# Kernel tuning notes

Measured on AMD Instinct MI355X. Metric: run time of the kernel, lower is better.

Reference implementation:

```python
import jax, jax.numpy as jnp
import numpy as np

S, B, D, H = 2048, 2, 1024, 16
DH = D // H
WINDOW = 256
DILATION = 1


def setup_inputs() -> dict:
    key = jax.random.key(0)
    ks = jax.random.split(key, 10)
    scale = 1.0 / np.sqrt(D)
    x = jax.random.normal(ks[0], (S, B, D), dtype=jnp.float32)
    Wq = jax.random.normal(ks[1], (D, D), dtype=jnp.float32) * scale
    Wk = jax.random.normal(ks[2], (D, D), dtype=jnp.float32) * scale
    Wv = jax.random.normal(ks[3], (D, D), dtype=jnp.float32) * scale
    Wo = jax.random.normal(ks[4], (D, D), dtype=jnp.float32) * scale
    bq = jax.random.normal(ks[5], (D,), dtype=jnp.float32) * 0.01
    bk = jax.random.normal(ks[6], (D,), dtype=jnp.float32) * 0.01
    bv = jax.random.normal(ks[7], (D,), dtype=jnp.float32) * 0.01
    bo = jax.random.normal(ks[8], (D,), dtype=jnp.float32) * 0.01
    beta = jax.random.normal(ks[9], (H,), dtype=jnp.float32) * 0.1
    return {"x": x, "Wq": Wq, "bq": bq, "Wk": Wk, "bk": bk,
            "Wv": Wv, "bv": bv, "Wo": Wo, "bo": bo, "beta": beta}


def _causal_window_bias(seq_len, window_len, dilation):
    # allowed iff 0 <= i-j <= dilation*(window_len-1) and (i-j) % dilation == 0
    idx = jnp.arange(seq_len)
    diff = idx[:, None] - idx[None, :]
    allowed = (diff >= 0) & (diff <= dilation * (window_len - 1)) & (diff % dilation == 0)
    return jnp.where(allowed, 0.0, -jnp.inf).astype(jnp.float32)  # [S, S]


def reference(x, Wq, bq, Wk, bk, Wv, bv, Wo, bo, beta):
    s, b, d = x.shape
    # projections (torch Linear: x @ W.T + b)
    q = x @ Wq.T + bq
    k = x @ Wk.T + bk
    v = x @ Wv.T + bv
    # 's b (h d) -> b h s d'
    q = q.reshape(s, b, H, DH).transpose(1, 2, 0, 3)
    k = k.reshape(s, b, H, DH).transpose(1, 2, 0, 3)
    v = v.reshape(s, b, H, DH).transpose(1, 2, 0, 3)
    # per-head beta scaling: q / (sqrt(d_head) * exp(beta))
    q = q / (np.sqrt(DH) * jnp.exp(beta)[None, :, None, None])
    bias = _causal_window_bias(s, WINDOW, DILATION)  # [S, S]
    scores = jnp.einsum('bhqd,bhkd->bhqk', q, k) + bias[None, None]
    p = jax.nn.softmax(scores, axis=-1)
    out = jnp.einsum('bhqk,bhkd->bhqd', p, v)
    # 'b h s d -> s b (h d)'
    out = out.transpose(2, 0, 1, 3).reshape(s, b, d)
    return out @ Wo.T + bo
```

## Files before the change

kernel.cpp:

```cpp
#include <hip/hip_runtime.h>
#include <hip/hip_bf16.h>

#define S_LEN 2048
#define BATCH 2
#define DMODEL 1024
#define NHEAD 16
#define DHEAD 64
#define WINDOW 256
#define MROWS (S_LEN * BATCH)

typedef unsigned short u16;
typedef unsigned int u32;
typedef __attribute__((ext_vector_type(8))) short bf16x8;
typedef __attribute__((ext_vector_type(4))) float f32x4;
typedef __attribute__((ext_vector_type(2))) unsigned int u32x2;

typedef const __attribute__((address_space(1))) void gvoid;
typedef __attribute__((address_space(3))) void lvoid;

__device__ __forceinline__ float b2f(u16 u) {
    union { unsigned int i; float f; } x; x.i = ((unsigned int)u) << 16; return x.f;
}
__device__ __forceinline__ u16 f2b(float f) {
    union { float f; unsigned int i; } x; x.f = f;
    unsigned int r = x.i + 0x7fffu + ((x.i >> 16) & 1u);
    return (u16)(r >> 16);
}
__device__ __forceinline__ u32 cvtpk(float a, float b) {
    u32 r; asm("v_cvt_pk_bf16_f32 %0, %1, %2" : "=v"(r) : "v"(a), "v"(b)); return r;
}
__device__ __forceinline__ bf16x8 ld8f(const float* __restrict__ p) {
    bf16x8 r;
    #pragma unroll
    for (int i = 0; i < 8; i++) r[i] = (short)f2b(p[i]);
    return r;
}
template<bool BF>
__device__ __forceinline__ bf16x8 ldrow(const void* __restrict__ base, size_t elemOff) {
    if constexpr (BF) return *reinterpret_cast<const bf16x8*>((const u16*)base + elemOff);
    else              return ld8f((const float*)base + elemOff);
}

__global__ __launch_bounds__(256) void cast_all(
    const float* __restrict__ x,  const float* __restrict__ Wq,
    const float* __restrict__ Wk, const float* __restrict__ Wv,
    const float* __restrict__ Wo,
    u16* __restrict__ xb, u16* __restrict__ wb, u16* __restrict__ wob)
{
    const size_t idx = ((size_t)blockIdx.x * 256 + threadIdx.x) * 8;
    const size_t M1 = 1048576;
    const float* src; u16* dst;
    if (idx < 4 * M1)      { src = x  + idx;            dst = xb  + idx; }
    else if (idx < 5 * M1) { src = Wq + (idx - 4 * M1); dst = wb  + (idx - 4 * M1); }
    else if (idx < 6 * M1) { src = Wk + (idx - 5 * M1); dst = wb  + (idx - 4 * M1); }
    else if (idx < 7 * M1) { src = Wv + (idx - 6 * M1); dst = wb  + (idx - 4 * M1); }
    else                   { src = Wo + (idx - 7 * M1); dst = wob + (idx - 7 * M1); }
    *reinterpret_cast<bf16x8*>(dst) = ld8f(src);
}

__global__ __launch_bounds__(256) void gemm_qkv_s(
    const u16* __restrict__ A, const u16* __restrict__ Wall,
    const float* __restrict__ bq, const float* __restrict__ bk, const float* __restrict__ bv,
    const float* __restrict__ beta,
    u16* __restrict__ qbuf, u16* __restrict__ kbuf, u16* __restrict__ vt)
{
    __shared__ u16 lA[128 * 32];
    __shared__ u16 lB[128 * 32];
    const int tid = threadIdx.x;
    const int lane = tid & 63, wave = tid >> 6;
    const int r15 = lane & 15, g = lane >> 4;
    const int m0 = blockIdx.x * 128;
    const int range = blockIdx.y >> 3;
    const int n0 = (blockIdx.y & 7) * 128;
    const u16* W = Wall + (size_t)range * DMODEL * DMODEL;
    const float* bias = (range == 0) ? bq : (range == 1) ? bk : bv;

    const int srow = tid >> 2;
    const int sslot = (tid & 3) ^ ((tid >> 3) & 3);
    const u16* aSrc = A + (size_t)(m0 + srow) * DMODEL + sslot * 8;
    const u16* wSrc = W + (size_t)(n0 + srow) * DMODEL + sslot * 8;
    const int ldsW = wave * 1024;
    const int mrow = (wave >> 1) * 64, nrow = (wave & 1) * 64;
    const int swz = (g ^ ((r15 >> 1) & 3)) << 4;
    const char* lAr = (const char*)lA + swz;
    const char* lBr = (const char*)lB + swz;

    f32x4 acc[4][4] = {};
    for (int kk = 0; kk < DMODEL; kk += 32) {
        __syncthreads();
        #pragma unroll
        for (int ro = 0; ro < 2; ro++) {
            __builtin_amdgcn_global_load_lds(
                (gvoid*)(aSrc + (size_t)ro * 64 * DMODEL + kk),
                (lvoid*)((char*)lA + ro * 4096 + ldsW), 16, 0, 0);
            __builtin_amdgcn_global_load_lds(
                (gvoid*)(wSrc + (size_t)ro * 64 * DMODEL + kk),
                (lvoid*)((char*)lB + ro * 4096 + ldsW), 16, 0, 0);
        }
        __syncthreads();
        bf16x8 af[4], bf[4];
        #pragma unroll
        for (int mi = 0; mi < 4; mi++)
            af[mi] = *reinterpret_cast<const bf16x8*>(lAr + ((mrow + mi * 16 + r15) << 6));
        #pragma unroll
        for (int ni = 0; ni < 4; ni++)
            bf[ni] = *reinterpret_cast<const bf16x8*>(lBr + ((nrow + ni * 16 + r15) << 6));
        #pragma unroll
        for (int mi = 0; mi < 4; mi++)
            #pragma unroll
            for (int ni = 0; ni < 4; ni++)
                acc[mi][ni] = __builtin_amdgcn_mfma_f32_16x16x32_bf16(
                    af[mi], bf[ni], acc[mi][ni], 0, 0, 0);
    }
    #pragma unroll
    for (int ni = 0; ni < 4; ni++) {
        const int col = n0 + nrow + ni * 16 + r15;
        const float bv_ = bias[col];
        float scale = 1.0f;
        if (range == 0) scale = 1.0f / (8.0f * __expf(beta[col >> 6]));
        #pragma unroll
        for (int mi = 0; mi < 4; mi++)
            #pragma unroll
            for (int r = 0; r < 4; r++) {
                const int row = m0 + mrow + mi * 16 + g * 4 + r;
                const float val = acc[mi][ni][r] + bv_;
                if (range == 0) {
                    qbuf[(size_t)row * DMODEL + col] = f2b(val * scale);
                } else if (range == 1) {
                    kbuf[(size_t)row * DMODEL + col] = f2b(val);
                } else {
                    const int b = row & 1, s = row >> 1;
                    vt[((size_t)(b * NHEAD + (col >> 6)) * DHEAD + (col & 63)) * S_LEN + s]
                        = f2b(val);
                }
            }
    }
}

__global__ __launch_bounds__(256) void gemm_out_s(
    const u16* __restrict__ A, const u16* __restrict__ W,
    const float* __restrict__ bias, float* __restrict__ C)
{
    __shared__ u16 lA[128 * 32];
    __shared__ u16 lB[128 * 32];
    const int tid = threadIdx.x;
    const int lane = tid & 63, wave = tid >> 6;
    const int r15 = lane & 15, g = lane >> 4;
    const int m0 = blockIdx.x * 128;
    const int n0 = blockIdx.y * 128;

    const int srow = tid >> 2;
    const int sslot = (tid & 3) ^ ((tid >> 3) & 3);
    const u16* aSrc = A + (size_t)(m0 + srow) * DMODEL + sslot * 8;
    const u16* wSrc = W + (size_t)(n0 + srow) * DMODEL + sslot * 8;
    const int ldsW = wave * 1024;
    const int mrow = (wave >> 1) * 64, nrow = (wave & 1) * 64;
    const int swz = (g ^ ((r15 >> 1) & 3)) << 4;
    const char* lAr = (const char*)lA + swz;
    const char* lBr = (const char*)lB + swz;

    f32x4 acc[4][4] = {};
    for (int kk = 0; kk < DMODEL; kk += 32) {
        __syncthreads();
        #pragma unroll
        for (int ro = 0; ro < 2; ro++) {
            __builtin_amdgcn_global_load_lds(
                (gvoid*)(aSrc + (size_t)ro * 64 * DMODEL + kk),
                (lvoid*)((char*)lA + ro * 4096 + ldsW), 16, 0, 0);
            __builtin_amdgcn_global_load_lds(
                (gvoid*)(wSrc + (size_t)ro * 64 * DMODEL + kk),
                (lvoid*)((char*)lB + ro * 4096 + ldsW), 16, 0, 0);
        }
        __syncthreads();
        bf16x8 af[4], bf[4];
        #pragma unroll
        for (int mi = 0; mi < 4; mi++)
            af[mi] = *reinterpret_cast<const bf16x8*>(lAr + ((mrow + mi * 16 + r15) << 6));
        #pragma unroll
        for (int ni = 0; ni < 4; ni++)
            bf[ni] = *reinterpret_cast<const bf16x8*>(lBr + ((nrow + ni * 16 + r15) << 6));
        #pragma unroll
        for (int mi = 0; mi < 4; mi++)
            #pragma unroll
            for (int ni = 0; ni < 4; ni++)
                acc[mi][ni] = __builtin_amdgcn_mfma_f32_16x16x32_bf16(
                    af[mi], bf[ni], acc[mi][ni], 0, 0, 0);
    }
    #pragma unroll
    for (int ni = 0; ni < 4; ni++) {
        const int col = n0 + nrow + ni * 16 + r15;
        const float bv_ = bias[col];
        #pragma unroll
        for (int mi = 0; mi < 4; mi++)
            #pragma unroll
            for (int r = 0; r < 4; r++) {
                const int row = m0 + mrow + mi * 16 + g * 4 + r;
                C[(size_t)row * DMODEL + col] = acc[mi][ni][r] + bv_;
            }
    }
}

template<bool ABF, bool WBF>
__global__ __launch_bounds__(256) void gemm_qkv_t(
    const void* __restrict__ A_,
    const void* __restrict__ Wq_, const void* __restrict__ Wk_, const void* __restrict__ Wv_,
    const float* __restrict__ bq, const float* __restrict__ bk, const float* __restrict__ bv,
    const float* __restrict__ beta,
    u16* __restrict__ qbuf, u16* __restrict__ kbuf, u16* __restrict__ vt)
{
    const int lane = threadIdx.x & 63;
    const int wave = threadIdx.x >> 6;
    const int r15 = lane & 15, g = lane >> 4;
    const int m0 = blockIdx.x * 128 + (wave >> 1) * 64;
    const int range = blockIdx.y >> 3;
    const int n0 = (blockIdx.y & 7) * 128 + (wave & 1) * 64;
    const void* W_ = (range == 0) ? Wq_ : (range == 1) ? Wk_ : Wv_;
    const float* bias = (range == 0) ? bq : (range == 1) ? bk : bv;
    const size_t aBase = (size_t)(m0 + r15) * DMODEL + g * 8;
    const size_t wBase = (size_t)(n0 + r15) * DMODEL + g * 8;
    f32x4 acc[4][4] = {};
    for (int k = 0; k < DMODEL; k += 32) {
        bf16x8 af[4], bf[4];
        #pragma unroll
        for (int mi = 0; mi < 4; mi++) af[mi] = ldrow<ABF>(A_, aBase + (size_t)mi * 16 * DMODEL + k);
        #pragma unroll
        for (int ni = 0; ni < 4; ni++) bf[ni] = ldrow<WBF>(W_, wBase + (size_t)ni * 16 * DMODEL + k);
        #pragma unroll
        for (int mi = 0; mi < 4; mi++)
            #pragma unroll
            for (int ni = 0; ni < 4; ni++)
                acc[mi][ni] = __builtin_amdgcn_mfma_f32_16x16x32_bf16(
                    af[mi], bf[ni], acc[mi][ni], 0, 0, 0);
    }
    #pragma unroll
    for (int ni = 0; ni < 4; ni++) {
        const int col = n0 + ni * 16 + r15;
        const float bv_ = bias[col];
        float scale = 1.0f;
        if (range == 0) scale = 1.0f / (8.0f * __expf(beta[col >> 6]));
        #pragma unroll
        for (int mi = 0; mi < 4; mi++)
            #pragma unroll
            for (int r = 0; r < 4; r++) {
                const int row = m0 + mi * 16 + g * 4 + r;
                const float val = acc[mi][ni][r] + bv_;
                if (range == 0) {
                    qbuf[(size_t)row * DMODEL + col] = f2b(val * scale);
                } else if (range == 1) {
                    kbuf[(size_t)row * DMODEL + col] = f2b(val);
                } else {
                    const int b = row & 1, s = row >> 1;
                    vt[((size_t)(b * NHEAD + (col >> 6)) * DHEAD + (col & 63)) * S_LEN + s]
                        = f2b(val);
                }
            }
    }
}

template<bool WBF>
__global__ __launch_bounds__(256) void gemm_out_t(
    const u16* __restrict__ A, const void* __restrict__ W_,
    const float* __restrict__ bias, float* __restrict__ C)
{
    const int lane = threadIdx.x & 63;
    const int wave = threadIdx.x >> 6;
    const int r15 = lane & 15, g = lane >> 4;
    const int m0 = blockIdx.x * 64 + (wave >> 1) * 32;
    const int n0 = blockIdx.y * 128 + (wave & 1) * 64;
    const u16* a0 = A + (size_t)(m0 + r15) * DMODEL + g * 8;
    const size_t wBase = (size_t)(n0 + r15) * DMODEL + g * 8;
    f32x4 acc[2][4] = {};
    for (int k = 0; k < DMODEL; k += 32) {
        bf16x8 af[2], bf[4];
        #pragma unroll
        for (int mi = 0; mi < 2; mi++)
            af[mi] = *reinterpret_cast<const bf16x8*>(a0 + (size_t)mi * 16 * DMODEL + k);
        #pragma unroll
        for (int ni = 0; ni < 4; ni++) bf[ni] = ldrow<WBF>(W_, wBase + (size_t)ni * 16 * DMODEL + k);
        #pragma unroll
        for (int mi = 0; mi < 2; mi++)
            #pragma unroll
            for (int ni = 0; ni < 4; ni++)
                acc[mi][ni] = __builtin_amdgcn_mfma_f32_16x16x32_bf16(
                    af[mi], bf[ni], acc[mi][ni], 0, 0, 0);
    }
    #pragma unroll
    for (int ni = 0; ni < 4; ni++) {
        const int col = n0 + ni * 16 + r15;
        const float bv_ = bias[col];
        #pragma unroll
        for (int mi = 0; mi < 2; mi++)
            #pragma unroll
            for (int r = 0; r < 4; r++) {
                const int row = m0 + mi * 16 + g * 4 + r;
                C[(size_t)row * DMODEL + col] = acc[mi][ni][r] + bv_;
            }
    }
}

__global__ __launch_bounds__(256) void attn3(
    const u16* __restrict__ qb, const u16* __restrict__ kb_,
    const u16* __restrict__ vt, u16* __restrict__ O)
{
    __shared__ u16 plds[4][16][64];
    const int lane = threadIdx.x & 63;
    const int wave = threadIdx.x >> 6;
    const int bid  = blockIdx.x;
    const int sbid = (bid & 7) * 128 + (bid >> 3);
    const int wid = sbid * 4 + wave;
    const int qt = wid & (S_LEN / 16 - 1);
    const int h  = (wid >> 7) & (NHEAD - 1);
    const int b  = wid >> 11;
    const int qstart = qt * 16;
    const int r15 = lane & 15, g = lane >> 4;
    const int i_glob = qstart + r15;

    const u16* qrow = qb + ((size_t)i_glob * BATCH + b) * DMODEL + h * DHEAD;
    const bf16x8 qf0 = *reinterpret_cast<const bf16x8*>(qrow + g * 8);
    const bf16x8 qf1 = *reinterpret_cast<const bf16x8*>(qrow + 32 + g * 8);
    const u16* vbase = vt + (size_t)(b * NHEAD + h) * DHEAD * S_LEN;

    char* prow = (char*)plds + wave * 2048 + r15 * 128;
    const int q7 = r15 & 7;

    float psum = 0.0f;
    f32x4 o[4] = {};
    const int kt0 = (qstart >= WINDOW) ? (qstart - WINDOW) : 0;

    for (int kt = kt0; kt <= qstart; kt += 64) {
        bf16x8 ka[4], kc[4];
        #pragma unroll
        for (int t = 0; t < 4; t++) {
            const int kr = min(kt + t * 16 + r15, S_LEN - 1);
            const u16* kp = kb_ + ((size_t)kr * BATCH + b) * DMODEL + h * DHEAD;
            ka[t] = *reinterpret_cast<const bf16x8*>(kp + g * 8);
            kc[t] = *reinterpret_cast<const bf16x8*>(kp + 32 + g * 8);
        }
        f32x4 st[4] = {};
        #pragma unroll
        for (int t = 0; t < 4; t++) {
            st[t] = __builtin_amdgcn_mfma_f32_16x16x32_bf16(ka[t], qf0, st[t], 0, 0, 0);
            st[t] = __builtin_amdgcn_mfma_f32_16x16x32_bf16(kc[t], qf1, st[t], 0, 0, 0);
        }

        #pragma unroll
        for (int t = 0; t < 4; t++) {
            float p[4];
            #pragma unroll
            for (int r = 0; r < 4; r++) {
                const int j = kt + t * 16 + g * 4 + r;
                const int d = i_glob - j;
                p[r] = (d < 0 || d >= WINDOW) ? 0.0f : __expf(st[t][r]);
                psum += p[r];
            }
            u32x2 w;
            w.x = cvtpk(p[0], p[1]);
            w.y = cvtpk(p[2], p[3]);
            *reinterpret_cast<u32x2*>(
                prow + ((((t << 1) + (g >> 1)) ^ q7) << 4) + ((g & 1) << 3)) = w;
        }

        const bf16x8 pf0 = *reinterpret_cast<const bf16x8*>(prow + ((g ^ q7) << 4));
        const bf16x8 pf1 = *reinterpret_cast<const bf16x8*>(prow + (((4 + g) ^ q7) << 4));

        int s0 = kt + g * 8;       if (s0 >= S_LEN) s0 = 0;
        int s1 = kt + 32 + g * 8;  if (s1 >= S_LEN) s1 = 0;
        #pragma unroll
        for (int c = 0; c < 4; c++) {
            const u16* vr = vbase + (size_t)(c * 16 + r15) * S_LEN;
            const bf16x8 vf0 = *reinterpret_cast<const bf16x8*>(vr + s0);
            const bf16x8 vf1 = *reinterpret_cast<const bf16x8*>(vr + s1);
            o[c] = __builtin_amdgcn_mfma_f32_16x16x32_bf16(vf0, pf0, o[c], 0, 0, 0);
            o[c] = __builtin_amdgcn_mfma_f32_16x16x32_bf16(vf1, pf1, o[c], 0, 0, 0);
        }
    }

    psum += __shfl_xor(psum, 16);
    psum += __shfl_xor(psum, 32);
    const float inv = 1.0f / psum;
    #pragma unroll
    for (int c = 0; c < 4; c++)
        #pragma unroll
        for (int r = 0; r < 4; r++) {
            const int dh = c * 16 + g * 4 + r;
            O[((size_t)i_glob * BATCH + b) * DMODEL + h * DHEAD + dh] = f2b(o[c][r] * inv);
        }
}

extern "C" void kernel_launch(void* const* d_in, const int* in_sizes, int n_in,
                              void* d_out, int out_size, void* d_ws, size_t ws_size,
                              hipStream_t stream) {
    const float* x    = (const float*)d_in[0];
    const float* Wq   = (const float*)d_in[1];
    const float* bq   = (const float*)d_in[2];
    const float* Wk   = (const float*)d_in[3];
    const float* bk   = (const float*)d_in[4];
    const float* Wv   = (const float*)d_in[5];
    const float* bv   = (const float*)d_in[6];
    const float* Wo   = (const float*)d_in[7];
    const float* bo   = (const float*)d_in[8];
    const float* beta = (const float*)d_in[9];
    float* out = (float*)d_out;
    u16* ws = (u16*)d_ws;

    const size_t M4 = (size_t)MROWS * DMODEL;
    u16* qbuf = (u16*)d_out;
    u16* kbuf = (u16*)d_out + M4;
    u16* vtb  = ws;
    u16* abuf = ws + M4;

    const int nattn = BATCH * NHEAD * (S_LEN / 16) / 4;
    dim3 gqkv(MROWS / 128, 24);
    dim3 gout(MROWS / 128, 8);

    if (ws_size >= (size_t)32 * 1024 * 1024) {
        u16* xb  = ws + 2 * M4;
        u16* wb  = ws + 3 * M4;
        u16* wob = ws + 3 * M4 + 3145728;
        cast_all<<<4096, 256, 0, stream>>>(x, Wq, Wk, Wv, Wo, xb, wb, wob);
        gemm_qkv_s<<<gqkv, 256, 0, stream>>>(xb, wb, bq, bk, bv, beta, qbuf, kbuf, vtb);
        attn3<<<nattn, 256, 0, stream>>>(qbuf, kbuf, vtb, abuf);
        gemm_out_s<<<gout, 256, 0, stream>>>(abuf, wob, bo, out);
    } else {
        dim3 gout2(MROWS / 64, 8);
        gemm_qkv_t<false, false><<<gqkv, 256, 0, stream>>>(
            x, Wq, Wk, Wv, bq, bk, bv, beta, qbuf, kbuf, vtb);
        attn3<<<nattn, 256, 0, stream>>>(qbuf, kbuf, vtb, abuf);
        gemm_out_t<false><<<gout2, 256, 0, stream>>>(abuf, Wo, bo, out);
    }
}
```

Before: 111.4 us.

## Split each attention query tile's key window across two waves and reduce via LDS

The attention kernel now assigns two waves to each 16-row query tile. Each wave processes up to three 64-key chunks of the 256-key window, and the partial outputs and softmax sums are combined through shared memory. This doubles the number of waves and shortens the serial per-wave loop to raise parallelism and latency hiding. In exchange it adds a block-wide barrier, an LDS reduction and extra clamped loads. An occupancy hint is also added to launch bounds.

After: 122.5 us. 1.1x slower.

```diff
diff --git a/kernel.cpp b/kernel.cpp
--- a/kernel.cpp
+++ b/kernel.cpp
@@ -298,19 +298,22 @@
     }
 }
 
-__global__ __launch_bounds__(256) void attn3(
+__global__ __launch_bounds__(256, 6) void attn4(
     const u16* __restrict__ qb, const u16* __restrict__ kb_,
     const u16* __restrict__ vt, u16* __restrict__ O)
 {
     __shared__ u16 plds[4][16][64];
+    __shared__ float ored[2][64][17];
     const int lane = threadIdx.x & 63;
     const int wave = threadIdx.x >> 6;
     const int bid  = blockIdx.x;
-    const int sbid = (bid & 7) * 128 + (bid >> 3);
-    const int wid = sbid * 4 + wave;
-    const int qt = wid & (S_LEN / 16 - 1);
-    const int h  = (wid >> 7) & (NHEAD - 1);
-    const int b  = wid >> 11;
+    const int sbid = (bid & 7) * 256 + (bid >> 3);
+    const int wid2 = sbid * 4 + wave;
+    const int half = wid2 & 1;
+    const int pair = wid2 >> 1;
+    const int qt = pair & (S_LEN / 16 - 1);
+    const int h  = (pair >> 7) & (NHEAD - 1);
+    const int b  = pair >> 11;
     const int qstart = qt * 16;
     const int r15 = lane & 15, g = lane >> 4;
     const int i_glob = qstart + r15;
@@ -325,66 +328,81 @@
 
     float psum = 0.0f;
     f32x4 o[4] = {};
-    const int kt0 = (qstart >= WINDOW) ? (qstart - WINDOW) : 0;
-
-    for (int kt = kt0; kt <= qstart; kt += 64) {
-        bf16x8 ka[4], kc[4];
-        #pragma unroll
-        for (int t = 0; t < 4; t++) {
-            const int kr = min(kt + t * 16 + r15, S_LEN - 1);
-            const u16* kp = kb_ + ((size_t)kr * BATCH + b) * DMODEL + h * DHEAD;
-            ka[t] = *reinterpret_cast<const bf16x8*>(kp + g * 8);
-            kc[t] = *reinterpret_cast<const bf16x8*>(kp + 32 + g * 8);
+
+    #pragma unroll
+    for (int i = 0; i < 3; i++) {
+        const int cs = qstart - WINDOW + (half * 3 + i) * 64;
+        if (cs >= -63 && cs <= qstart) {
+            bf16x8 ka[4], kc[4];
+            #pragma unroll
+            for (int t = 0; t < 4; t++) {
+                const int kr = min(max(cs + t * 16 + r15, 0), S_LEN - 1);
+                const u16* kp = kb_ + ((size_t)kr * BATCH + b) * DMODEL + h * DHEAD;
+                ka[t] = *reinterpret_cast<const bf16x8*>(kp + g * 8);
+                kc[t] = *reinterpret_cast<const bf16x8*>(kp + 32 + g * 8);
+            }
+            f32x4 st[4] = {};
+            #pragma unroll
+            for (int t = 0; t < 4; t++) {
+                st[t] = __builtin_amdgcn_mfma_f32_16x16x32_bf16(ka[t], qf0, st[t], 0, 0, 0);
+                st[t] = __builtin_amdgcn_mfma_f32_16x16x32_bf16(kc[t], qf1, st[t], 0, 0, 0);
+            }
+            #pragma unroll
+            for (int t = 0; t < 4; t++) {
+                float p[4];
+                #pragma unroll
+                for (int r = 0; r < 4; r++) {
+                    const int j = cs + t * 16 + g * 4 + r;
+                    const int d = i_glob - j;
+                    p[r] = (j < 0 || d < 0 || d >= WINDOW) ? 0.0f : __expf(st[t][r]);
+                    psum += p[r];
+                }
+                u32x2 w;
+                w.x = cvtpk(p[0], p[1]);
+                w.y = cvtpk(p[2], p[3]);
+                *reinterpret_cast<u32x2*>(
+                    prow + ((((t << 1) + (g >> 1)) ^ q7) << 4) + ((g & 1) << 3)) = w;
+            }
+            const bf16x8 pf0 = *reinterpret_cast<const bf16x8*>(prow + ((g ^ q7) << 4));
+            const bf16x8 pf1 = *reinterpret_cast<const bf16x8*>(prow + (((4 + g) ^ q7) << 4));
+            const int s0 = min(max(cs + g * 8, 0), S_LEN - 8);
+            const int s1 = min(max(cs + 32 + g * 8, 0), S_LEN - 8);
+            #pragma unroll
+            for (int c = 0; c < 4; c++) {
+                const u16* vr = vbase + (size_t)(c * 16 + r15) * S_LEN;
+                const bf16x8 vf0 = *reinterpret_cast<const bf16x8*>(vr + s0);
+                const bf16x8 vf1 = *reinterpret_cast<const bf16x8*>(vr + s1);
+                o[c] = __builtin_amdgcn_mfma_f32_16x16x32_bf16(vf0, pf0, o[c], 0, 0, 0);
+                o[c] = __builtin_amdgcn_mfma_f32_16x16x32_bf16(vf1, pf1, o[c], 0, 0, 0);
+            }
         }
-        f32x4 st[4] = {};
-        #pragma unroll
-        for (int t = 0; t < 4; t++) {
-            st[t] = __builtin_amdgcn_mfma_f32_16x16x32_bf16(ka[t], qf0, st[t], 0, 0, 0);
-            st[t] = __builtin_amdgcn_mfma_f32_16x16x32_bf16(kc[t], qf1, st[t], 0, 0, 0);
-        }
-
-        #pragma unroll
-        for (int t = 0; t < 4; t++) {
-            float p[4];
+    }
+
+    if (half) {
+        #pragma unroll
+        for (int c = 0; c < 4; c++)
+            #pragma unroll
+            for (int r = 0; r < 4; r++) ored[wave >> 1][lane][c * 4 + r] = o[c][r];
+        ored[wave >> 1][lane][16] = psum;
+    }
+    __syncthreads();
+    if (!half) {
+        #pragma unroll
+        for (int c = 0; c < 4; c++)
+            #pragma unroll
+            for (int r = 0; r < 4; r++) o[c][r] += ored[wave >> 1][lane][c * 4 + r];
+        psum += ored[wave >> 1][lane][16];
+        psum += __shfl_xor(psum, 16);
+        psum += __shfl_xor(psum, 32);
+        const float inv = 1.0f / psum;
+        #pragma unroll
+        for (int c = 0; c < 4; c++)
             #pragma unroll
             for (int r = 0; r < 4; r++) {
-                const int j = kt + t * 16 + g * 4 + r;
-                const int d = i_glob - j;
-                p[r] = (d < 0 || d >= WINDOW) ? 0.0f : __expf(st[t][r]);
-                psum += p[r];
-            }
-            u32x2 w;
-            w.x = cvtpk(p[0], p[1]);
-            w.y = cvtpk(p[2], p[3]);
-            *reinterpret_cast<u32x2*>(
-                prow + ((((t << 1) + (g >> 1)) ^ q7) << 4) + ((g & 1) << 3)) = w;
-        }
-
-        const bf16x8 pf0 = *reinterpret_cast<const bf16x8*>(prow + ((g ^ q7) << 4));
-        const bf16x8 pf1 = *reinterpret_cast<const bf16x8*>(prow + (((4 + g) ^ q7) << 4));
-
-        int s0 = kt + g * 8;       if (s0 >= S_LEN) s0 = 0;
-        int s1 = kt + 32 + g * 8;  if (s1 >= S_LEN) s1 = 0;
-        #pragma unroll
-        for (int c = 0; c < 4; c++) {
-            const u16* vr = vbase + (size_t)(c * 16 + r15) * S_LEN;
-            const bf16x8 vf0 = *reinterpret_cast<const bf16x8*>(vr + s0);
-            const bf16x8 vf1 = *reinterpret_cast<const bf16x8*>(vr + s1);
-            o[c] = __builtin_amdgcn_mfma_f32_16x16x32_bf16(vf0, pf0, o[c], 0, 0, 0);
-            o[c] = __builtin_amdgcn_mfma_f32_16x16x32_bf16(vf1, pf1, o[c], 0, 0, 0);
-        }
-    }
-
-    psum += __shfl_xor(psum, 16);
-    psum += __shfl_xor(psum, 32);
-    const float inv = 1.0f / psum;
-    #pragma unroll
-    for (int c = 0; c < 4; c++)
-        #pragma unroll
-        for (int r = 0; r < 4; r++) {
-            const int dh = c * 16 + g * 4 + r;
-            O[((size_t)i_glob * BATCH + b) * DMODEL + h * DHEAD + dh] = f2b(o[c][r] * inv);
-        }
+                const int dh = c * 16 + g * 4 + r;
+                O[((size_t)i_glob * BATCH + b) * DMODEL + h * DHEAD + dh] = f2b(o[c][r] * inv);
+            }
+    }
 }
 
 extern "C" void kernel_launch(void* const* d_in, const int* in_sizes, int n_in,
@@ -409,7 +427,7 @@
     u16* vtb  = ws;
     u16* abuf = ws + M4;
 
-    const int nattn = BATCH * NHEAD * (S_LEN / 16) / 4;
+    const int nattn = BATCH * NHEAD * (S_LEN / 16) * 2 / 4;
     dim3 gqkv(MROWS / 128, 24);
     dim3 gout(MROWS / 128, 8);
 
@@ -419,13 +437,13 @@
         u16* wob = ws + 3 * M4 + 3145728;
         cast_all<<<4096, 256, 0, stream>>>(x, Wq, Wk, Wv, Wo, xb, wb, wob);
         gemm_qkv_s<<<gqkv, 256, 0, stream>>>(xb, wb, bq, bk, bv, beta, qbuf, kbuf, vtb);
-        attn3<<<nattn, 256, 0, stream>>>(qbuf, kbuf, vtb, abuf);
+        attn4<<<nattn, 256, 0, stream>>>(qbuf, kbuf, vtb, abuf);
         gemm_out_s<<<gout, 256, 0, stream>>>(abuf, wob, bo, out);
     } else {
         dim3 gout2(MROWS / 64, 8);
         gemm_qkv_t<false, false><<<gqkv, 256, 0, stream>>>(
             x, Wq, Wk, Wv, bq, bk, bv, beta, qbuf, kbuf, vtb);
-        attn3<<<nattn, 256, 0, stream>>>(qbuf, kbuf, vtb, abuf);
+        attn4<<<nattn, 256, 0, stream>>>(qbuf, kbuf, vtb, abuf);
         gemm_out_t<false><<<gout2, 256, 0, stream>>>(abuf, Wo, bo, out);
     }
 }
```

## Swizzle global bf16 layouts across all stages and double-buffer attention P tile

Applied to the files above, without the earlier changes.

Applies an XOR swizzle on 128-element chunks, keyed by row, to the global layouts of the bf16 x/weights, Q, K, V^T and the attention output. Every producer and consumer kernel is updated to match, so row-strided global accesses are spread across memory channels instead of colliding. The attention P scratch in LDS is also double-buffered by key-tile parity, which may relax the ordering between writing and reading P. The cost is extra index math and a layout coupling that every stage must keep consistent. The non-workspace fallback path keeps the unswizzled layout.

New measurement: 132.2 us. 18.7% more time.

```diff
diff --git a/kernel.cpp b/kernel.cpp
--- a/kernel.cpp
+++ b/kernel.cpp
@@ -49,14 +49,16 @@
 {
     const size_t idx = ((size_t)blockIdx.x * 256 + threadIdx.x) * 8;
     const size_t M1 = 1048576;
+    const size_t sw = ((idx >> 10) & 7) << 7;
     const float* src; u16* dst;
-    if (idx < 4 * M1)      { src = x  + idx;            dst = xb  + idx; }
-    else if (idx < 5 * M1) { src = Wq + (idx - 4 * M1); dst = wb  + (idx - 4 * M1); }
-    else if (idx < 6 * M1) { src = Wk + (idx - 5 * M1); dst = wb  + (idx - 4 * M1); }
-    else if (idx < 7 * M1) { src = Wv + (idx - 6 * M1); dst = wb  + (idx - 4 * M1); }
-    else                   { src = Wo + (idx - 7 * M1); dst = wob + (idx - 7 * M1); }
+    if (idx < 4 * M1)      { src = x  + idx;            dst = xb  + ((idx)          ^ sw); }
+    else if (idx < 5 * M1) { src = Wq + (idx - 4 * M1); dst = wb  + ((idx - 4 * M1) ^ sw); }
+    else if (idx < 6 * M1) { src = Wk + (idx - 5 * M1); dst = wb  + ((idx - 4 * M1) ^ sw); }
+    else if (idx < 7 * M1) { src = Wv + (idx - 6 * M1); dst = wb  + ((idx - 4 * M1) ^ sw); }
+    else                   { src = Wo + (idx - 7 * M1); dst = wob + ((idx - 7 * M1) ^ sw); }
     *reinterpret_cast<bf16x8*>(dst) = ld8f(src);
 }
+
 
 __global__ __launch_bounds__(256) void gemm_qkv_s(
     const u16* __restrict__ A, const u16* __restrict__ Wall,
@@ -77,6 +79,7 @@
 
     const int srow = tid >> 2;
     const int sslot = (tid & 3) ^ ((tid >> 3) & 3);
+    const int arswz = ((srow & 7) << 7);
     const u16* aSrc = A + (size_t)(m0 + srow) * DMODEL + sslot * 8;
     const u16* wSrc = W + (size_t)(n0 + srow) * DMODEL + sslot * 8;
     const int ldsW = wave * 1024;
@@ -87,14 +90,15 @@
 
     f32x4 acc[4][4] = {};
     for (int kk = 0; kk < DMODEL; kk += 32) {
+        const int kks = kk ^ arswz;
         __syncthreads();
         #pragma unroll
         for (int ro = 0; ro < 2; ro++) {
             __builtin_amdgcn_global_load_lds(
-                (gvoid*)(aSrc + (size_t)ro * 64 * DMODEL + kk),
+                (gvoid*)(aSrc + (size_t)ro * 64 * DMODEL + kks),
                 (lvoid*)((char*)lA + ro * 4096 + ldsW), 16, 0, 0);
             __builtin_amdgcn_global_load_lds(
-                (gvoid*)(wSrc + (size_t)ro * 64 * DMODEL + kk),
+                (gvoid*)(wSrc + (size_t)ro * 64 * DMODEL + kks),
                 (lvoid*)((char*)lB + ro * 4096 + ldsW), 16, 0, 0);
         }
         __syncthreads();
@@ -123,15 +127,16 @@
             #pragma unroll
             for (int r = 0; r < 4; r++) {
                 const int row = m0 + mrow + mi * 16 + g * 4 + r;
+                const int s = row >> 1;
                 const float val = acc[mi][ni][r] + bv_;
                 if (range == 0) {
-                    qbuf[(size_t)row * DMODEL + col] = f2b(val * scale);
+                    qbuf[(size_t)row * DMODEL + (col ^ ((s & 7) << 7))] = f2b(val * scale);
                 } else if (range == 1) {
-                    kbuf[(size_t)row * DMODEL + col] = f2b(val);
+                    kbuf[(size_t)row * DMODEL + (col ^ ((s & 7) << 7))] = f2b(val);
                 } else {
-                    const int b = row & 1, s = row >> 1;
-                    vt[((size_t)(b * NHEAD + (col >> 6)) * DHEAD + (col & 63)) * S_LEN + s]
-                        = f2b(val);
+                    const int b = row & 1;
+                    vt[((size_t)(b * NHEAD + (col >> 6)) * DHEAD + (col & 63)) * S_LEN
+                       + (s ^ ((col & 7) << 7))] = f2b(val);
                 }
             }
     }
@@ -151,6 +156,7 @@
 
     const int srow = tid >> 2;
     const int sslot = (tid & 3) ^ ((tid >> 3) & 3);
+    const int arswz = ((srow & 7) << 7);
     const u16* aSrc = A + (size_t)(m0 + srow) * DMODEL + sslot * 8;
     const u16* wSrc = W + (size_t)(n0 + srow) * DMODEL + sslot * 8;
     const int ldsW = wave * 1024;
@@ -161,14 +167,15 @@
 
     f32x4 acc[4][4] = {};
     for (int kk = 0; kk < DMODEL; kk += 32) {
+        const int kks = kk ^ arswz;
         __syncthreads();
         #pragma unroll
         for (int ro = 0; ro < 2; ro++) {
             __builtin_amdgcn_global_load_lds(
-                (gvoid*)(aSrc + (size_t)ro * 64 * DMODEL + kk),
+                (gvoid*)(aSrc + (size_t)ro * 64 * DMODEL + kks),
                 (lvoid*)((char*)lA + ro * 4096 + ldsW), 16, 0, 0);
             __builtin_amdgcn_global_load_lds(
-                (gvoid*)(wSrc + (size_t)ro * 64 * DMODEL + kk),
+                (gvoid*)(wSrc + (size_t)ro * 64 * DMODEL + kks),
                 (lvoid*)((char*)lB + ro * 4096 + ldsW), 16, 0, 0);
         }
         __syncthreads();
@@ -298,11 +305,12 @@
     }
 }
 
-__global__ __launch_bounds__(256) void attn3(
+template<bool SWZ>
+__global__ __launch_bounds__(256) void attn5(
     const u16* __restrict__ qb, const u16* __restrict__ kb_,
     const u16* __restrict__ vt, u16* __restrict__ O)
 {
-    __shared__ u16 plds[4][16][64];
+    __shared__ u16 plds[2][4][16][64];
     const int lane = threadIdx.x & 63;
     const int wave = threadIdx.x >> 6;
     const int bid  = blockIdx.x;
@@ -314,25 +322,26 @@
     const int qstart = qt * 16;
     const int r15 = lane & 15, g = lane >> 4;
     const int i_glob = qstart + r15;
-
-    const u16* qrow = qb + ((size_t)i_glob * BATCH + b) * DMODEL + h * DHEAD;
+    const int sw7 = SWZ ? ((r15 & 7) << 7) : 0;
+
+    const u16* qrow = qb + ((size_t)i_glob * BATCH + b) * DMODEL + ((h * DHEAD) ^ sw7);
     const bf16x8 qf0 = *reinterpret_cast<const bf16x8*>(qrow + g * 8);
     const bf16x8 qf1 = *reinterpret_cast<const bf16x8*>(qrow + 32 + g * 8);
     const u16* vbase = vt + (size_t)(b * NHEAD + h) * DHEAD * S_LEN;
 
-    char* prow = (char*)plds + wave * 2048 + r15 * 128;
     const int q7 = r15 & 7;
-
     float psum = 0.0f;
     f32x4 o[4] = {};
     const int kt0 = (qstart >= WINDOW) ? (qstart - WINDOW) : 0;
 
     for (int kt = kt0; kt <= qstart; kt += 64) {
+        char* prow = (char*)plds + (((kt >> 6) & 1) << 13) + wave * 2048 + r15 * 128;
         bf16x8 ka[4], kc[4];
         #pragma unroll
         for (int t = 0; t < 4; t++) {
             const int kr = min(kt + t * 16 + r15, S_LEN - 1);
-            const u16* kp = kb_ + ((size_t)kr * BATCH + b) * DMODEL + h * DHEAD;
+            const u16* kp = kb_ + ((size_t)kr * BATCH + b) * DMODEL
+                          + ((h * DHEAD) ^ (SWZ ? ((kr & 7) << 7) : 0));
             ka[t] = *reinterpret_cast<const bf16x8*>(kp + g * 8);
             kc[t] = *reinterpret_cast<const bf16x8*>(kp + 32 + g * 8);
         }
@@ -342,7 +351,6 @@
             st[t] = __builtin_amdgcn_mfma_f32_16x16x32_bf16(ka[t], qf0, st[t], 0, 0, 0);
             st[t] = __builtin_amdgcn_mfma_f32_16x16x32_bf16(kc[t], qf1, st[t], 0, 0, 0);
         }
-
         #pragma unroll
         for (int t = 0; t < 4; t++) {
             float p[4];
@@ -359,17 +367,15 @@
             *reinterpret_cast<u32x2*>(
                 prow + ((((t << 1) + (g >> 1)) ^ q7) << 4) + ((g & 1) << 3)) = w;
         }
-
         const bf16x8 pf0 = *reinterpret_cast<const bf16x8*>(prow + ((g ^ q7) << 4));
         const bf16x8 pf1 = *reinterpret_cast<const bf16x8*>(prow + (((4 + g) ^ q7) << 4));
-
         int s0 = kt + g * 8;       if (s0 >= S_LEN) s0 = 0;
         int s1 = kt + 32 + g * 8;  if (s1 >= S_LEN) s1 = 0;
         #pragma unroll
         for (int c = 0; c < 4; c++) {
             const u16* vr = vbase + (size_t)(c * 16 + r15) * S_LEN;
-            const bf16x8 vf0 = *reinterpret_cast<const bf16x8*>(vr + s0);
-            const bf16x8 vf1 = *reinterpret_cast<const bf16x8*>(vr + s1);
+            const bf16x8 vf0 = *reinterpret_cast<const bf16x8*>(vr + (s0 ^ sw7));
+            const bf16x8 vf1 = *reinterpret_cast<const bf16x8*>(vr + (s1 ^ sw7));
             o[c] = __builtin_amdgcn_mfma_f32_16x16x32_bf16(vf0, pf0, o[c], 0, 0, 0);
             o[c] = __builtin_amdgcn_mfma_f32_16x16x32_bf16(vf1, pf1, o[c], 0, 0, 0);
         }
@@ -378,12 +384,14 @@
     psum += __shfl_xor(psum, 16);
     psum += __shfl_xor(psum, 32);
     const float inv = 1.0f / psum;
+    const int orow = i_glob * BATCH + b;
+    const int osw = SWZ ? ((orow & 7) << 7) : 0;
     #pragma unroll
     for (int c = 0; c < 4; c++)
         #pragma unroll
         for (int r = 0; r < 4; r++) {
             const int dh = c * 16 + g * 4 + r;
-            O[((size_t)i_glob * BATCH + b) * DMODEL + h * DHEAD + dh] = f2b(o[c][r] * inv);
+            O[(size_t)orow * DMODEL + ((h * DHEAD + dh) ^ osw)] = f2b(o[c][r] * inv);
         }
 }
 
@@ -419,13 +427,13 @@
         u16* wob = ws + 3 * M4 + 3145728;
         cast_all<<<4096, 256, 0, stream>>>(x, Wq, Wk, Wv, Wo, xb, wb, wob);
         gemm_qkv_s<<<gqkv, 256, 0, stream>>>(xb, wb, bq, bk, bv, beta, qbuf, kbuf, vtb);
-        attn3<<<nattn, 256, 0, stream>>>(qbuf, kbuf, vtb, abuf);
+        attn5<true><<<nattn, 256, 0, stream>>>(qbuf, kbuf, vtb, abuf);
         gemm_out_s<<<gout, 256, 0, stream>>>(abuf, wob, bo, out);
     } else {
         dim3 gout2(MROWS / 64, 8);
         gemm_qkv_t<false, false><<<gqkv, 256, 0, stream>>>(
             x, Wq, Wk, Wv, bq, bk, bv, beta, qbuf, kbuf, vtb);
-        attn3<<<nattn, 256, 0, stream>>>(qbuf, kbuf, vtb, abuf);
+        attn5<false><<<nattn, 256, 0, stream>>>(qbuf, kbuf, vtb, abuf);
         gemm_out_t<false><<<gout2, 256, 0, stream>>>(abuf, Wo, bo, out);
     }
 }
```

## Share K/V tiles in LDS across the four waves of an attention block

Applied to the files above, without the earlier changes.

Rewrites the sliding-window attention kernel so each block's four waves cover four consecutive 16-row query tiles of the same head. K and V tiles of 64 keys are loaded cooperatively into swizzled LDS with global_load_lds and shared across the waves, instead of each wave loading its own K/V from global memory. Each block now iterates over up to five 64-key chunks, with masking extended to cover negative key indices. This cuts redundant global/L2 traffic in exchange for two barriers per chunk and a slightly larger common key range per wave (5 chunks versus about 4-5 per wave).

Result: faster. 93.08 us, median of 2 (-16.4%).

```diff
diff --git a/kernel.cpp b/kernel.cpp
--- a/kernel.cpp
+++ b/kernel.cpp
@@ -298,19 +298,22 @@
     }
 }
 
-__global__ __launch_bounds__(256) void attn3(
+__global__ __launch_bounds__(256) void attn6(
     const u16* __restrict__ qb, const u16* __restrict__ kb_,
     const u16* __restrict__ vt, u16* __restrict__ O)
 {
+    __shared__ u16 lK[64 * 64];
+    __shared__ u16 lV[64 * 64];
     __shared__ u16 plds[4][16][64];
-    const int lane = threadIdx.x & 63;
-    const int wave = threadIdx.x >> 6;
+    const int tid  = threadIdx.x;
+    const int lane = tid & 63;
+    const int wave = tid >> 6;
     const int bid  = blockIdx.x;
     const int sbid = (bid & 7) * 128 + (bid >> 3);
-    const int wid = sbid * 4 + wave;
-    const int qt = wid & (S_LEN / 16 - 1);
-    const int h  = (wid >> 7) & (NHEAD - 1);
-    const int b  = wid >> 11;
+    const int qblk = sbid & 31;
+    const int h    = (sbid >> 5) & (NHEAD - 1);
+    const int b    = sbid >> 9;
+    const int qt = qblk * 4 + wave;
     const int qstart = qt * 16;
     const int r15 = lane & 15, g = lane >> 4;
     const int i_glob = qstart + r15;
@@ -318,29 +321,47 @@
     const u16* qrow = qb + ((size_t)i_glob * BATCH + b) * DMODEL + h * DHEAD;
     const bf16x8 qf0 = *reinterpret_cast<const bf16x8*>(qrow + g * 8);
     const bf16x8 qf1 = *reinterpret_cast<const bf16x8*>(qrow + 32 + g * 8);
-    const u16* vbase = vt + (size_t)(b * NHEAD + h) * DHEAD * S_LEN;
 
     char* prow = (char*)plds + wave * 2048 + r15 * 128;
     const int q7 = r15 & 7;
 
+    const int sr_lo = wave * 8 + (lane >> 3);
+    const int scol8 = lane & 7;
+
     float psum = 0.0f;
     f32x4 o[4] = {};
-    const int kt0 = (qstart >= WINDOW) ? (qstart - WINDOW) : 0;
-
-    for (int kt = kt0; kt <= qstart; kt += 64) {
-        bf16x8 ka[4], kc[4];
+
+    #pragma unroll
+    for (int c = 0; c < 5; c++) {
+        const int kstart = qblk * 64 - WINDOW + c * 64;
+        if (kstart < -63) continue;
+
+        __syncthreads();
+        #pragma unroll
+        for (int i = 0; i < 2; i++) {
+            const int srow = i * 32 + sr_lo;
+            const int sc = scol8 ^ (srow & 7);
+            const int ks = min(max(kstart + srow, 0), S_LEN - 1);
+            __builtin_amdgcn_global_load_lds(
+                (gvoid*)(kb_ + ((size_t)ks * BATCH + b) * DMODEL + h * DHEAD + sc * 8),
+                (lvoid*)((char*)lK + i * 4096 + wave * 1024), 16, 0, 0);
+            const int vs = min(max(kstart + sc * 8, 0), S_LEN - 8);
+            __builtin_amdgcn_global_load_lds(
+                (gvoid*)(vt + ((size_t)(b * NHEAD + h) * DHEAD + srow) * S_LEN + vs),
+                (lvoid*)((char*)lV + i * 4096 + wave * 1024), 16, 0, 0);
+        }
+        __syncthreads();
+
+        f32x4 st[4] = {};
         #pragma unroll
         for (int t = 0; t < 4; t++) {
-            const int kr = min(kt + t * 16 + r15, S_LEN - 1);
-            const u16* kp = kb_ + ((size_t)kr * BATCH + b) * DMODEL + h * DHEAD;
-            ka[t] = *reinterpret_cast<const bf16x8*>(kp + g * 8);
-            kc[t] = *reinterpret_cast<const bf16x8*>(kp + 32 + g * 8);
-        }
-        f32x4 st[4] = {};
-        #pragma unroll
-        for (int t = 0; t < 4; t++) {
-            st[t] = __builtin_amdgcn_mfma_f32_16x16x32_bf16(ka[t], qf0, st[t], 0, 0, 0);
-            st[t] = __builtin_amdgcn_mfma_f32_16x16x32_bf16(kc[t], qf1, st[t], 0, 0, 0);
+            const int R = t * 16 + r15;
+            const bf16x8 ka = *reinterpret_cast<const bf16x8*>(
+                lK + R * 64 + ((g ^ (R & 7)) << 3));
+            const bf16x8 kc = *reinterpret_cast<const bf16x8*>(
+                lK + R * 64 + (((4 + g) ^ (R & 7)) << 3));
+            st[t] = __builtin_amdgcn_mfma_f32_16x16x32_bf16(ka, qf0, st[t], 0, 0, 0);
+            st[t] = __builtin_amdgcn_mfma_f32_16x16x32_bf16(kc, qf1, st[t], 0, 0, 0);
         }
 
         #pragma unroll
@@ -348,9 +369,9 @@
             float p[4];
             #pragma unroll
             for (int r = 0; r < 4; r++) {
-                const int j = kt + t * 16 + g * 4 + r;
+                const int j = kstart + t * 16 + g * 4 + r;
                 const int d = i_glob - j;
-                p[r] = (d < 0 || d >= WINDOW) ? 0.0f : __expf(st[t][r]);
+                p[r] = (j < 0 || d < 0 || d >= WINDOW) ? 0.0f : __expf(st[t][r]);
                 psum += p[r];
             }
             u32x2 w;
@@ -359,19 +380,18 @@
             *reinterpret_cast<u32x2*>(
                 prow + ((((t << 1) + (g >> 1)) ^ q7) << 4) + ((g & 1) << 3)) = w;
         }
-
         const bf16x8 pf0 = *reinterpret_cast<const bf16x8*>(prow + ((g ^ q7) << 4));
         const bf16x8 pf1 = *reinterpret_cast<const bf16x8*>(prow + (((4 + g) ^ q7) << 4));
 
-        int s0 = kt + g * 8;       if (s0 >= S_LEN) s0 = 0;
-        int s1 = kt + 32 + g * 8;  if (s1 >= S_LEN) s1 = 0;
-        #pragma unroll
-        for (int c = 0; c < 4; c++) {
-            const u16* vr = vbase + (size_t)(c * 16 + r15) * S_LEN;
-            const bf16x8 vf0 = *reinterpret_cast<const bf16x8*>(vr + s0);
-            const bf16x8 vf1 = *reinterpret_cast<const bf16x8*>(vr + s1);
-            o[c] = __builtin_amdgcn_mfma_f32_16x16x32_bf16(vf0, pf0, o[c], 0, 0, 0);
-            o[c] = __builtin_amdgcn_mfma_f32_16x16x32_bf16(vf1, pf1, o[c], 0, 0, 0);
+        #pragma unroll
+        for (int c4 = 0; c4 < 4; c4++) {
+            const int R = c4 * 16 + r15;
+            const bf16x8 vf0 = *reinterpret_cast<const bf16x8*>(
+                lV + R * 64 + ((g ^ (R & 7)) << 3));
+            const bf16x8 vf1 = *reinterpret_cast<const bf16x8*>(
+                lV + R * 64 + (((4 + g) ^ (R & 7)) << 3));
+            o[c4] = __builtin_amdgcn_mfma_f32_16x16x32_bf16(vf0, pf0, o[c4], 0, 0, 0);
+            o[c4] = __builtin_amdgcn_mfma_f32_16x16x32_bf16(vf1, pf1, o[c4], 0, 0, 0);
         }
     }
 
@@ -379,11 +399,11 @@
     psum += __shfl_xor(psum, 32);
     const float inv = 1.0f / psum;
     #pragma unroll
-    for (int c = 0; c < 4; c++)
+    for (int c4 = 0; c4 < 4; c4++)
         #pragma unroll
         for (int r = 0; r < 4; r++) {
-            const int dh = c * 16 + g * 4 + r;
-            O[((size_t)i_glob * BATCH + b) * DMODEL + h * DHEAD + dh] = f2b(o[c][r] * inv);
+            const int dh = c4 * 16 + g * 4 + r;
+            O[((size_t)i_glob * BATCH + b) * DMODEL + h * DHEAD + dh] = f2b(o[c4][r] * inv);
         }
 }
 
@@ -409,7 +429,7 @@
     u16* vtb  = ws;
     u16* abuf = ws + M4;
 
-    const int nattn = BATCH * NHEAD * (S_LEN / 16) / 4;
+    const int nattn = BATCH * NHEAD * (S_LEN / 64);
     dim3 gqkv(MROWS / 128, 24);
     dim3 gout(MROWS / 128, 8);
 
@@ -419,13 +439,13 @@
         u16* wob = ws + 3 * M4 + 3145728;
         cast_all<<<4096, 256, 0, stream>>>(x, Wq, Wk, Wv, Wo, xb, wb, wob);
         gemm_qkv_s<<<gqkv, 256, 0, stream>>>(xb, wb, bq, bk, bv, beta, qbuf, kbuf, vtb);
-        attn3<<<nattn, 256, 0, stream>>>(qbuf, kbuf, vtb, abuf);
+        attn6<<<nattn, 256, 0, stream>>>(qbuf, kbuf, vtb, abuf);
         gemm_out_s<<<gout, 256, 0, stream>>>(abuf, wob, bo, out);
     } else {
         dim3 gout2(MROWS / 64, 8);
         gemm_qkv_t<false, false><<<gqkv, 256, 0, stream>>>(
             x, Wq, Wk, Wv, bq, bk, bv, beta, qbuf, kbuf, vtb);
-        attn3<<<nattn, 256, 0, stream>>>(qbuf, kbuf, vtb, abuf);
+        attn6<<<nattn, 256, 0, stream>>>(qbuf, kbuf, vtb, abuf);
         gemm_out_t<false><<<gout2, 256, 0, stream>>>(abuf, Wo, bo, out);
     }
 }
```
